# Kernel optimization log

Hardware: AMD Instinct MI355X
Metric: run time of the kernel (lower is better)

The kernel has to match this reference:

```python
import jax, jax.numpy as jnp
import numpy as np

HIDDEN = 896
N_HEADS = 14
N_KV_HEADS = 2
HEAD_DIM = HIDDEN // N_HEADS  # 64
KV_GROUPS = N_HEADS // N_KV_HEADS  # 7
ROPE_THETA = 1000000.0


def rotate_half(x):
    x1, x2 = x[..., : x.shape[-1] // 2], x[..., x.shape[-1] // 2 :]
    return jnp.concatenate((-x2, x1), axis=-1)


def rope_tables(seq_len, dtype=jnp.float32):
    inv_freq = 1.0 / (ROPE_THETA ** (jnp.arange(0, HEAD_DIM, 2, dtype=jnp.float32) / HEAD_DIM))
    t = jnp.arange(seq_len, dtype=jnp.float32)
    freqs = jnp.outer(t, inv_freq)            # [S, D/2]
    emb = jnp.concatenate((freqs, freqs), -1)  # [S, D]
    return jnp.cos(emb).astype(dtype), jnp.sin(emb).astype(dtype)


def setup_inputs() -> dict:
    key = jax.random.key(0)
    ks = jax.random.split(key, 8)
    B, S = 2, 2048
    s = 0.02
    return {
        "hidden_states": jax.random.normal(ks[0], (B, S, HIDDEN), jnp.float32),
        "wq": jax.random.normal(ks[1], (HIDDEN, N_HEADS * HEAD_DIM), jnp.float32) * s,
        "bq": jnp.zeros((N_HEADS * HEAD_DIM,), jnp.float32),
        "wk": jax.random.normal(ks[2], (HIDDEN, N_KV_HEADS * HEAD_DIM), jnp.float32) * s,
        "bk": jnp.zeros((N_KV_HEADS * HEAD_DIM,), jnp.float32),
        "wv": jax.random.normal(ks[3], (HIDDEN, N_KV_HEADS * HEAD_DIM), jnp.float32) * s,
        "bv": jnp.zeros((N_KV_HEADS * HEAD_DIM,), jnp.float32),
        "wo": jax.random.normal(ks[4], (N_HEADS * HEAD_DIM, HIDDEN), jnp.float32) * s,
    }


def reference(hidden_states, wq, bq, wk, bk, wv, bv, wo):
    B, S, _ = hidden_states.shape
    q = (hidden_states @ wq + bq).reshape(B, S, N_HEADS, HEAD_DIM)
    k = (hidden_states @ wk + bk).reshape(B, S, N_KV_HEADS, HEAD_DIM)
    v = (hidden_states @ wv + bv).reshape(B, S, N_KV_HEADS, HEAD_DIM)

    cos, sin = rope_tables(S, hidden_states.dtype)
    cos, sin = cos[None, :, None, :], sin[None, :, None, :]
    q = q * cos + rotate_half(q) * sin
    k = k * cos + rotate_half(k) * sin

    # GQA broadcast: repeat kv heads to match query heads
    k = jnp.repeat(k, KV_GROUPS, axis=2)
    v = jnp.repeat(v, KV_GROUPS, axis=2)

    # [B, H, S, S]
    scores = jnp.einsum("bqhd,bkhd->bhqk", q, k) / jnp.sqrt(jnp.asarray(HEAD_DIM, hidden_states.dtype))
    mask = jnp.tril(jnp.ones((S, S), dtype=jnp.bool_))
    scores = jnp.where(mask[None, None, :, :], scores, jnp.asarray(-1e9, scores.dtype))
    attn = jax.nn.softmax(scores, axis=-1)
    out = jnp.einsum("bhqk,bkhd->bqhd", attn, v).reshape(B, S, N_HEADS * HEAD_DIM)
    return out @ wo
```

## Files before the change

kernel.cpp:

```cpp
#include <hip/hip_runtime.h>

#define HID 896
#define NQ 896
#define NKV 128
#define NQKV 1152
#define NH 14
#define NKVH 2
#define GQ 7
#define DH 64
#define SEQ 2048
#define BATCH 2
#define TOK (BATCH*SEQ)

typedef __attribute__((ext_vector_type(8))) short short8;
typedef __attribute__((ext_vector_type(4))) float f32x4;
typedef __attribute__((ext_vector_type(4))) unsigned short us4;

__device__ __forceinline__ unsigned short f2bf(float x) {
  unsigned int u = __builtin_bit_cast(unsigned int, x);
  u = (u + 0x7fffu + ((u >> 16) & 1u)) >> 16;
  return (unsigned short)u;
}
__device__ __forceinline__ float bf2f(unsigned short b) {
  return __builtin_bit_cast(float, (unsigned int)b << 16);
}
__device__ __forceinline__ f32x4 fzero4() {
  f32x4 z; z[0]=0.f; z[1]=0.f; z[2]=0.f; z[3]=0.f; return z;
}
__device__ __forceinline__ unsigned int cvt_pk_bf16(float lo, float hi) {
  unsigned int r;
  asm("v_cvt_pk_bf16_f32 %0, %1, %2" : "=v"(r) : "v"(lo), "v"(hi));
  return r;
}
__device__ __forceinline__ void gload_lds16(const unsigned short* g, unsigned short* l) {
  __builtin_amdgcn_global_load_lds(
      (const __attribute__((address_space(1))) void*)(const void*)g,
      (__attribute__((address_space(3))) void*)(void*)l, 16, 0, 0);
}

#define CVT_BLKS 3584
#define TRN_BLKS 448
#define BIAS_BLKS 5
#define TAB_BLKS 256
#define PREP_BLKS (CVT_BLKS + TRN_BLKS + BIAS_BLKS + TAB_BLKS)

__global__ void k_prep(const float* __restrict__ hs,
                       const float* __restrict__ wq, const float* __restrict__ bq,
                       const float* __restrict__ wk, const float* __restrict__ bk,
                       const float* __restrict__ wv, const float* __restrict__ bv,
                       const float* __restrict__ wo,
                       unsigned short* __restrict__ hb,
                       unsigned short* __restrict__ wqkvt,
                       unsigned short* __restrict__ wot,
                       float* __restrict__ bqkv,
                       float* __restrict__ ct, float* __restrict__ st) {
  __shared__ unsigned short Ls[64*65];
  int blk = blockIdx.x, tid = threadIdx.x;
  if (blk < CVT_BLKS) {
    int i = blk*256 + tid;
    float4 v = ((const float4*)hs)[i];
    us4 o; o[0]=f2bf(v.x); o[1]=f2bf(v.y); o[2]=f2bf(v.z); o[3]=f2bf(v.w);
    ((us4*)hb)[i] = o;
    return;
  }
  blk -= CVT_BLKS;
  if (blk < TRN_BLKS) {
    const float* W; unsigned short* out; int K, N, n0, k0;
    if (blk < 196)      { W=wq; out=wqkvt;                        K=HID; N=NQ;  int t=blk;     n0=(t%14)*64; k0=(t/14)*64; }
    else if (blk < 224) { W=wk; out=wqkvt + (size_t)NQ*HID;       K=HID; N=NKV; int t=blk-196; n0=(t%2)*64;  k0=(t/2)*64; }
    else if (blk < 252) { W=wv; out=wqkvt + (size_t)(NQ+NKV)*HID; K=HID; N=NKV; int t=blk-224; n0=(t%2)*64;  k0=(t/2)*64; }
    else                { W=wo; out=wot;                          K=NQ;  N=HID; int t=blk-252; n0=(t%14)*64; k0=(t/14)*64; }
    #pragma unroll
    for (int i = 0; i < 16; ++i) {
      int idx = i*256 + tid;
      int r = idx >> 6, c = idx & 63;
      Ls[c*65 + r] = f2bf(W[(size_t)(k0 + r)*N + n0 + c]);
    }
    __syncthreads();
    #pragma unroll
    for (int i = 0; i < 16; ++i) {
      int idx = i*256 + tid;
      int r2 = idx >> 6, c2 = idx & 63;
      out[(size_t)(n0 + r2)*K + k0 + c2] = Ls[r2*65 + c2];
    }
    return;
  }
  blk -= TRN_BLKS;
  if (blk < BIAS_BLKS) {
    int i = blk*256 + tid;
    if (i < NQKV) {
      if (i < NQ) bqkv[i] = bq[i];
      else if (i < NQ + NKV) bqkv[i] = bk[i - NQ];
      else bqkv[i] = bv[i - NQ - NKV];
    }
    return;
  }
  blk -= BIAS_BLKS;
  {
    int i = blk*256 + tid;
    int s = i >> 5, dp = i & 31;
    float inv = __expf(-(float)(2*dp) * (13.815510557964274f / 64.0f));
    float f = (float)s * inv;
    ct[i] = cosf(f); st[i] = sinf(f);
  }
}

template<int OUTMODE>
__global__ __launch_bounds__(256, 2) void k_gemm_bt(
    const unsigned short* __restrict__ A,
    const unsigned short* __restrict__ Bt,
    const float* __restrict__ bias,
    void* __restrict__ Cout,
    int M, int N, int K) {
  __shared__ unsigned short As[128*64];
  __shared__ unsigned short Bs[128*64];
  int tid = threadIdx.x;
  int lane = tid & 63, w = tid >> 6;
  int wr = w >> 1, wc = w & 1;
  int l15 = lane & 15, l4 = lane >> 4;
  int m0 = blockIdx.y * 128, n0 = blockIdx.x * 128;

  f32x4 acc[4][4];
  #pragma unroll
  for (int i = 0; i < 4; ++i)
    #pragma unroll
    for (int j = 0; j < 4; ++j) acc[i][j] = fzero4();

  int nkt = K >> 6;
  for (int kt = 0; kt < nkt; ++kt) {
    int k0 = kt << 6;
    #pragma unroll
    for (int t = 0; t < 4; ++t) {
      int chunk = t*256 + w*64 + lane;
      int row = chunk >> 3, sp = chunk & 7;
      int sl = sp ^ (row & 7);
      gload_lds16(A + (size_t)(m0+row)*K + k0 + sl*8, &As[(t*256 + w*64)*8]);
      gload_lds16(Bt + (size_t)(n0+row)*K + k0 + sl*8, &Bs[(t*256 + w*64)*8]);
    }
    __syncthreads();
    #pragma unroll
    for (int s = 0; s < 2; ++s) {
      short8 af[4], bfr[4];
      #pragma unroll
      for (int mi = 0; mi < 4; ++mi) {
        int row = wr*64 + mi*16 + l15;
        int slot = (s*4 + l4) ^ (row & 7);
        af[mi] = *reinterpret_cast<const short8*>(&As[row*64 + slot*8]);
      }
      #pragma unroll
      for (int ni = 0; ni < 4; ++ni) {
        int row = wc*64 + ni*16 + l15;
        int slot = (s*4 + l4) ^ (row & 7);
        bfr[ni] = *reinterpret_cast<const short8*>(&Bs[row*64 + slot*8]);
      }
      #pragma unroll
      for (int mi = 0; mi < 4; ++mi)
        #pragma unroll
        for (int ni = 0; ni < 4; ++ni)
          acc[mi][ni] = __builtin_amdgcn_mfma_f32_16x16x32_bf16(af[mi], bfr[ni], acc[mi][ni], 0, 0, 0);
    }
    __syncthreads();
  }
  #pragma unroll
  for (int mi = 0; mi < 4; ++mi) {
    #pragma unroll
    for (int ni = 0; ni < 4; ++ni) {
      #pragma unroll
      for (int r = 0; r < 4; ++r) {
        int row = m0 + wr*64 + mi*16 + l4*4 + r;
        int col = n0 + wc*64 + ni*16 + l15;
        float v = acc[mi][ni][r];
        if (OUTMODE == 0) {
          v += bias[col];
          ((unsigned short*)Cout)[(size_t)row*N + col] = f2bf(v);
        } else {
          ((float*)Cout)[(size_t)row*N + col] = v;
        }
      }
    }
  }
}

__global__ void k_rope(const unsigned short* __restrict__ qkv,
                       const float* __restrict__ ct, const float* __restrict__ st,
                       unsigned short* __restrict__ Qr, unsigned short* __restrict__ Kr,
                       unsigned short* __restrict__ Vt) {
  int t = blockIdx.x; int b = t >> 11; int s = t & 2047;
  int tid = threadIdx.x;
  const unsigned short* row = qkv + (size_t)t * NQKV;
  if (tid < 448) {
    int h = tid >> 5, dp = tid & 31;
    float x1 = bf2f(row[h*64 + dp]);
    float x2 = bf2f(row[h*64 + dp + 32]);
    float c = ct[s*32 + dp], sn = st[s*32 + dp];
    size_t base = (((size_t)b*NH + h)*SEQ + s)*64;
    Qr[base + dp]      = f2bf((x1*c - x2*sn) * 0.125f);
    Qr[base + dp + 32] = f2bf((x2*c + x1*sn) * 0.125f);
  } else {
    int j = tid - 448;
    int kvh = j >> 5, dp = j & 31;
    float x1 = bf2f(row[NQ + kvh*64 + dp]);
    float x2 = bf2f(row[NQ + kvh*64 + dp + 32]);
    float c = ct[s*32 + dp], sn = st[s*32 + dp];
    size_t base = (((size_t)b*NKVH + kvh)*SEQ + s)*64;
    Kr[base + dp]      = f2bf(x1*c - x2*sn);
    Kr[base + dp + 32] = f2bf(x2*c + x1*sn);
  }
  if (tid < 128) {
    int kvh = tid >> 6, d = tid & 63;
    Vt[(((size_t)b*NKVH + kvh)*64 + d)*SEQ + s] = row[1024 + kvh*64 + d];
  }
}

__global__ __launch_bounds__(512, 2) void k_attn(
    const unsigned short* __restrict__ Q,
    const unsigned short* __restrict__ Kr,
    const unsigned short* __restrict__ Vt,
    unsigned short* __restrict__ Aout) {
  __shared__ __align__(16) unsigned short Kst[2][64*64];
  __shared__ __align__(16) unsigned short Vst[2][64*64];
  __shared__ __align__(16) unsigned short P_lds[8][16*64];
  int lane = threadIdx.x & 63, w = threadIdx.x >> 6;
  int grp = w >> 2, wsub = w & 3;
  int l15 = lane & 15, l4 = lane >> 4;
  int i = blockIdx.x, h = blockIdx.y, b = blockIdx.z;
  int qtH = 31 - i, qtL = i;
  int qt = grp ? qtL : qtH;
  int kvh = h / GQ;
  const unsigned short* Kb = Kr + ((size_t)(b*NKVH + kvh))*SEQ*64;
  const unsigned short* Vb = Vt + ((size_t)(b*NKVH + kvh))*64*SEQ;
  char* Pw = (char*)&P_lds[w][0];

  auto stage = [&](int kt, int bsel) {
    int chunk = w*64 + lane;
    int row = chunk >> 3;
    int sl = (chunk & 7) ^ (row & 7);
    gload_lds16(Kb + (size_t)(kt*64 + row)*64 + sl*8, &Kst[bsel][chunk*8]);
    gload_lds16(Vb + (size_t)row*SEQ + kt*64 + sl*8, &Vst[bsel][chunk*8]);
  };

  const unsigned short* Qb = Q + (((size_t)(b*NH + h))*SEQ + qt*64 + wsub*16) * 64;
  short8 qa[2];
  #pragma unroll
  for (int s = 0; s < 2; ++s)
    qa[s] = *reinterpret_cast<const short8*>(Qb + l15*64 + s*32 + l4*8);

  f32x4 acc[4];
  #pragma unroll
  for (int n = 0; n < 4; ++n) acc[n] = fzero4();
  float m_run = -__builtin_inff(), l_run = 0.0f;

  stage(0, 0);
  __syncthreads();
  int cur = 0;
  int nkt = qtH + 1;

  for (int kt = 0; kt < nkt; ++kt) {
    if (kt + 1 < nkt) stage(kt + 1, cur ^ 1);
    if (kt <= qt) {
      f32x4 sa[4];
      #pragma unroll
      for (int n = 0; n < 4; ++n) sa[n] = fzero4();
      __builtin_amdgcn_s_setprio(1);
      #pragma unroll
      for (int s = 0; s < 2; ++s) {
        short8 kb[4];
        #pragma unroll
        for (int n = 0; n < 4; ++n) {
          int row = n*16 + l15;
          int slot = (s*4 + l4) ^ (row & 7);
          kb[n] = *reinterpret_cast<const short8*>(&Kst[cur][row*64 + slot*8]);
        }
        #pragma unroll
        for (int n = 0; n < 4; ++n)
          sa[n] = __builtin_amdgcn_mfma_f32_16x16x32_bf16(kb[n], qa[s], sa[n], 0, 0, 0);
      }
      __builtin_amdgcn_s_setprio(0);
      if (kt == qt) {
        int q_glob = qt*64 + wsub*16 + l15;
        #pragma unroll
        for (int n = 0; n < 4; ++n)
          #pragma unroll
          for (int r = 0; r < 4; ++r) {
            int kpos = kt*64 + n*16 + l4*4 + r;
            if (kpos > q_glob) sa[n][r] = -1e30f;
          }
      }
      float t0 = fmaxf(fmaxf(sa[0][0],sa[0][1]), fmaxf(sa[0][2],sa[0][3]));
      float t1 = fmaxf(fmaxf(sa[1][0],sa[1][1]), fmaxf(sa[1][2],sa[1][3]));
      float t2 = fmaxf(fmaxf(sa[2][0],sa[2][1]), fmaxf(sa[2][2],sa[2][3]));
      float t3 = fmaxf(fmaxf(sa[3][0],sa[3][1]), fmaxf(sa[3][2],sa[3][3]));
      float tmax = fmaxf(fmaxf(t0,t1), fmaxf(t2,t3));
      tmax = fmaxf(tmax, __shfl_xor(tmax, 16));
      tmax = fmaxf(tmax, __shfl_xor(tmax, 32));
      float mn = fmaxf(m_run, tmax);
      float sc = __expf(m_run - mn);
      #pragma unroll
      for (int n = 0; n < 4; ++n)
        #pragma unroll
        for (int r = 0; r < 4; ++r) sa[n][r] = __expf(sa[n][r] - mn);
      float s0 = (sa[0][0]+sa[0][1]) + (sa[0][2]+sa[0][3]);
      float s1 = (sa[1][0]+sa[1][1]) + (sa[1][2]+sa[1][3]);
      float s2 = (sa[2][0]+sa[2][1]) + (sa[2][2]+sa[2][3]);
      float s3 = (sa[3][0]+sa[3][1]) + (sa[3][2]+sa[3][3]);
      float sum = (s0+s1) + (s2+s3);
      sum += __shfl_xor(sum, 16);
      sum += __shfl_xor(sum, 32);
      m_run = mn;
      l_run = l_run*sc + sum;
      #pragma unroll
      for (int n = 0; n < 4; ++n) acc[n] *= sc;
      #pragma unroll
      for (int n = 0; n < 4; ++n) {
        uint2 pk;
        pk.x = cvt_pk_bf16(sa[n][0], sa[n][1]);
        pk.y = cvt_pk_bf16(sa[n][2], sa[n][3]);
        int colbyte = n*32 + l4*8;
        int addr = l15*128 + ((((colbyte>>4) ^ (l15&7))) << 4) + (colbyte & 15);
        *reinterpret_cast<uint2*>(Pw + addr) = pk;
      }
      __builtin_amdgcn_s_setprio(1);
      #pragma unroll
      for (int s2i = 0; s2i < 2; ++s2i) {
        int pslot = (s2i*4 + l4) ^ (l15 & 7);
        short8 pa = *reinterpret_cast<const short8*>(Pw + l15*128 + pslot*16);
        #pragma unroll
        for (int n = 0; n < 4; ++n) {
          int row = n*16 + l15;
          int vslot = (s2i*4 + l4) ^ (row & 7);
          short8 vb = *reinterpret_cast<const short8*>(&Vst[cur][row*64 + vslot*8]);
          acc[n] = __builtin_amdgcn_mfma_f32_16x16x32_bf16(vb, pa, acc[n], 0, 0, 0);
        }
      }
      __builtin_amdgcn_s_setprio(0);
    }
    __syncthreads();
    cur ^= 1;
  }

  float inv = 1.0f / l_run;
  #pragma unroll
  for (int n = 0; n < 4; ++n) {
    uint2 pk;
    pk.x = cvt_pk_bf16(acc[n][0]*inv, acc[n][1]*inv);
    pk.y = cvt_pk_bf16(acc[n][2]*inv, acc[n][3]*inv);
    int colbyte = n*32 + l4*8;
    int addr = l15*128 + ((((colbyte>>4) ^ (l15&7))) << 4) + (colbyte & 15);
    *reinterpret_cast<uint2*>(Pw + addr) = pk;
  }
  int row = lane >> 2;
  int cb0 = (lane & 3) * 32;
  #pragma unroll
  for (int it = 0; it < 2; ++it) {
    int cb = cb0 + it*16;
    int slot = (cb >> 4) ^ (row & 7);
    short8 v = *reinterpret_cast<const short8*>(Pw + row*128 + slot*16);
    size_t tok = (size_t)b*SEQ + qt*64 + wsub*16 + row;
    *reinterpret_cast<short8*>(&Aout[tok*NQ + h*64 + (cb>>1)]) = v;
  }
}

extern "C" void kernel_launch(void* const* d_in, const int* in_sizes, int n_in,
                              void* d_out, int out_size, void* d_ws, size_t ws_size,
                              hipStream_t stream) {
  const float* hs = (const float*)d_in[0];
  const float* wq = (const float*)d_in[1];
  const float* bq = (const float*)d_in[2];
  const float* wk = (const float*)d_in[3];
  const float* bk = (const float*)d_in[4];
  const float* wv = (const float*)d_in[5];
  const float* bv = (const float*)d_in[6];
  const float* wo = (const float*)d_in[7];
  float* out = (float*)d_out;

  char* p = (char*)d_ws;
  auto alloc = [&](size_t bytes) { char* r = p; p += (bytes + 255) & ~(size_t)255; return r; };
  unsigned short* hb    = (unsigned short*)alloc((size_t)TOK*HID*2);
  unsigned short* wqkvt = (unsigned short*)alloc((size_t)NQKV*HID*2);
  unsigned short* wot   = (unsigned short*)alloc((size_t)HID*NQ*2);
  float*          bqkv  = (float*)alloc(NQKV*4);
  unsigned short* qkvt  = (unsigned short*)alloc((size_t)TOK*NQKV*2);
  unsigned short* q_r   = (unsigned short*)alloc((size_t)BATCH*NH*SEQ*DH*2);
  unsigned short* k_r   = (unsigned short*)alloc((size_t)BATCH*NKVH*SEQ*DH*2);
  unsigned short* v_t   = (unsigned short*)alloc((size_t)BATCH*NKVH*DH*SEQ*2);
  float*          ct    = (float*)alloc((size_t)SEQ*32*4);
  float*          st    = (float*)alloc((size_t)SEQ*32*4);
  unsigned short* attn  = hb;

  k_prep<<<PREP_BLKS, 256, 0, stream>>>(hs, wq, bq, wk, bk, wv, bv, wo,
                                        hb, wqkvt, wot, bqkv, ct, st);
  k_gemm_bt<0><<<dim3(NQKV/128, TOK/128), 256, 0, stream>>>(hb, wqkvt, bqkv, qkvt, TOK, NQKV, HID);
  k_rope<<<TOK, 512, 0, stream>>>(qkvt, ct, st, q_r, k_r, v_t);
  k_attn<<<dim3(16, NH, BATCH), 512, 0, stream>>>(q_r, k_r, v_t, attn);
  k_gemm_bt<1><<<dim3(NQ/128, TOK/128), 256, 0, stream>>>(attn, wot, nullptr, out, TOK, NQ, HID);
}
```

Baseline: 103.3 us.

## Stage two KV tiles per barrier in attention loop to halve syncs

The attention kernel now loads K/V in slabs of two 64-key tiles per pipeline stage, double-buffered, and processes both tiles between barriers. This halves the number of __syncthreads and makes each prefetch larger, so more work overlaps each global-to-LDS load. In exchange LDS use doubles (K/V buffers go from 32KB to 64KB), which may limit the two blocks per CU implied by the launch bounds. For odd tile counts it also loads one redundant clamped tile.

```diff
diff --git a/kernel.cpp b/kernel.cpp
--- a/kernel.cpp
+++ b/kernel.cpp
@@ -217,8 +217,8 @@
     const unsigned short* __restrict__ Kr,
     const unsigned short* __restrict__ Vt,
     unsigned short* __restrict__ Aout) {
-  __shared__ __align__(16) unsigned short Kst[2][64*64];
-  __shared__ __align__(16) unsigned short Vst[2][64*64];
+  __shared__ __align__(16) unsigned short Kst[2][2][64*64];
+  __shared__ __align__(16) unsigned short Vst[2][2][64*64];
   __shared__ __align__(16) unsigned short P_lds[8][16*64];
   int lane = threadIdx.x & 63, w = threadIdx.x >> 6;
   int grp = w >> 2, wsub = w & 3;
@@ -231,12 +231,16 @@
   const unsigned short* Vb = Vt + ((size_t)(b*NKVH + kvh))*64*SEQ;
   char* Pw = (char*)&P_lds[w][0];
 
-  auto stage = [&](int kt, int bsel) {
-    int chunk = w*64 + lane;
-    int row = chunk >> 3;
-    int sl = (chunk & 7) ^ (row & 7);
-    gload_lds16(Kb + (size_t)(kt*64 + row)*64 + sl*8, &Kst[bsel][chunk*8]);
-    gload_lds16(Vb + (size_t)row*SEQ + kt*64 + sl*8, &Vst[bsel][chunk*8]);
+  auto stage = [&](int slab, int bsel) {
+    #pragma unroll
+    for (int t = 0; t < 2; ++t) {
+      int ks = slab*2 + t; if (ks > 31) ks = 31;
+      int chunk = w*64 + lane;
+      int row = chunk >> 3;
+      int sl = (chunk & 7) ^ (row & 7);
+      gload_lds16(Kb + (size_t)(ks*64 + row)*64 + sl*8, &Kst[bsel][t][chunk*8]);
+      gload_lds16(Vb + (size_t)row*SEQ + ks*64 + sl*8, &Vst[bsel][t][chunk*8]);
+    }
   };
 
   const unsigned short* Qb = Q + (((size_t)(b*NH + h))*SEQ + qt*64 + wsub*16) * 64;
@@ -254,85 +258,92 @@
   __syncthreads();
   int cur = 0;
   int nkt = qtH + 1;
-
-  for (int kt = 0; kt < nkt; ++kt) {
-    if (kt + 1 < nkt) stage(kt + 1, cur ^ 1);
-    if (kt <= qt) {
-      f32x4 sa[4];
-      #pragma unroll
-      for (int n = 0; n < 4; ++n) sa[n] = fzero4();
-      __builtin_amdgcn_s_setprio(1);
-      #pragma unroll
-      for (int s = 0; s < 2; ++s) {
-        short8 kb[4];
-        #pragma unroll
-        for (int n = 0; n < 4; ++n) {
-          int row = n*16 + l15;
-          int slot = (s*4 + l4) ^ (row & 7);
-          kb[n] = *reinterpret_cast<const short8*>(&Kst[cur][row*64 + slot*8]);
+  int nslab = (nkt + 1) >> 1;
+
+  for (int s = 0; s < nslab; ++s) {
+    if (s + 1 < nslab) stage(s + 1, cur ^ 1);
+    #pragma unroll
+    for (int t = 0; t < 2; ++t) {
+      int ks = s*2 + t;
+      if (ks <= qt) {
+        const unsigned short* Ks = &Kst[cur][t][0];
+        const unsigned short* Vs = &Vst[cur][t][0];
+        f32x4 sa[4];
+        #pragma unroll
+        for (int n = 0; n < 4; ++n) sa[n] = fzero4();
+        __builtin_amdgcn_s_setprio(1);
+        #pragma unroll
+        for (int si = 0; si < 2; ++si) {
+          short8 kb[4];
+          #pragma unroll
+          for (int n = 0; n < 4; ++n) {
+            int row = n*16 + l15;
+            int slot = (si*4 + l4) ^ (row & 7);
+            kb[n] = *reinterpret_cast<const short8*>(&Ks[row*64 + slot*8]);
+          }
+          #pragma unroll
+          for (int n = 0; n < 4; ++n)
+            sa[n] = __builtin_amdgcn_mfma_f32_16x16x32_bf16(kb[n], qa[si], sa[n], 0, 0, 0);
         }
-        #pragma unroll
-        for (int n = 0; n < 4; ++n)
-          sa[n] = __builtin_amdgcn_mfma_f32_16x16x32_bf16(kb[n], qa[s], sa[n], 0, 0, 0);
-      }
-      __builtin_amdgcn_s_setprio(0);
-      if (kt == qt) {
-        int q_glob = qt*64 + wsub*16 + l15;
+        __builtin_amdgcn_s_setprio(0);
+        if (ks == qt) {
+          int q_glob = qt*64 + wsub*16 + l15;
+          #pragma unroll
+          for (int n = 0; n < 4; ++n)
+            #pragma unroll
+            for (int r = 0; r < 4; ++r) {
+              int kpos = ks*64 + n*16 + l4*4 + r;
+              if (kpos > q_glob) sa[n][r] = -1e30f;
+            }
+        }
+        float t0 = fmaxf(fmaxf(sa[0][0],sa[0][1]), fmaxf(sa[0][2],sa[0][3]));
+        float t1 = fmaxf(fmaxf(sa[1][0],sa[1][1]), fmaxf(sa[1][2],sa[1][3]));
+        float t2 = fmaxf(fmaxf(sa[2][0],sa[2][1]), fmaxf(sa[2][2],sa[2][3]));
+        float t3 = fmaxf(fmaxf(sa[3][0],sa[3][1]), fmaxf(sa[3][2],sa[3][3]));
+        float tmax = fmaxf(fmaxf(t0,t1), fmaxf(t2,t3));
+        tmax = fmaxf(tmax, __shfl_xor(tmax, 16));
+        tmax = fmaxf(tmax, __shfl_xor(tmax, 32));
+        float mn = fmaxf(m_run, tmax);
+        float sc = __expf(m_run - mn);
         #pragma unroll
         for (int n = 0; n < 4; ++n)
           #pragma unroll
-          for (int r = 0; r < 4; ++r) {
-            int kpos = kt*64 + n*16 + l4*4 + r;
-            if (kpos > q_glob) sa[n][r] = -1e30f;
+          for (int r = 0; r < 4; ++r) sa[n][r] = __expf(sa[n][r] - mn);
+        float s0 = (sa[0][0]+sa[0][1]) + (sa[0][2]+sa[0][3]);
+        float s1 = (sa[1][0]+sa[1][1]) + (sa[1][2]+sa[1][3]);
+        float s2 = (sa[2][0]+sa[2][1]) + (sa[2][2]+sa[2][3]);
+        float s3 = (sa[3][0]+sa[3][1]) + (sa[3][2]+sa[3][3]);
+        float sum = (s0+s1) + (s2+s3);
+        sum += __shfl_xor(sum, 16);
+        sum += __shfl_xor(sum, 32);
+        m_run = mn;
+        l_run = l_run*sc + sum;
+        #pragma unroll
+        for (int n = 0; n < 4; ++n) acc[n] *= sc;
+        #pragma unroll
+        for (int n = 0; n < 4; ++n) {
+          uint2 pk;
+          pk.x = cvt_pk_bf16(sa[n][0], sa[n][1]);
+          pk.y = cvt_pk_bf16(sa[n][2], sa[n][3]);
+          int colbyte = n*32 + l4*8;
+          int addr = l15*128 + ((((colbyte>>4) ^ (l15&7))) << 4) + (colbyte & 15);
+          *reinterpret_cast<uint2*>(Pw + addr) = pk;
+        }
+        __builtin_amdgcn_s_setprio(1);
+        #pragma unroll
+        for (int s2i = 0; s2i < 2; ++s2i) {
+          int pslot = (s2i*4 + l4) ^ (l15 & 7);
+          short8 pa = *reinterpret_cast<const short8*>(Pw + l15*128 + pslot*16);
+          #pragma unroll
+          for (int n = 0; n < 4; ++n) {
+            int row = n*16 + l15;
+            int vslot = (s2i*4 + l4) ^ (row & 7);
+            short8 vb = *reinterpret_cast<const short8*>(&Vs[row*64 + vslot*8]);
+            acc[n] = __builtin_amdgcn_mfma_f32_16x16x32_bf16(vb, pa, acc[n], 0, 0, 0);
           }
+        }
+        __builtin_amdgcn_s_setprio(0);
       }
-      float t0 = fmaxf(fmaxf(sa[0][0],sa[0][1]), fmaxf(sa[0][2],sa[0][3]));
-      float t1 = fmaxf(fmaxf(sa[1][0],sa[1][1]), fmaxf(sa[1][2],sa[1][3]));
-      float t2 = fmaxf(fmaxf(sa[2][0],sa[2][1]), fmaxf(sa[2][2],sa[2][3]));
-      float t3 = fmaxf(fmaxf(sa[3][0],sa[3][1]), fmaxf(sa[3][2],sa[3][3]));
-      float tmax = fmaxf(fmaxf(t0,t1), fmaxf(t2,t3));
-      tmax = fmaxf(tmax, __shfl_xor(tmax, 16));
-      tmax = fmaxf(tmax, __shfl_xor(tmax, 32));
-      float mn = fmaxf(m_run, tmax);
-      float sc = __expf(m_run - mn);
-      #pragma unroll
-      for (int n = 0; n < 4; ++n)
-        #pragma unroll
-        for (int r = 0; r < 4; ++r) sa[n][r] = __expf(sa[n][r] - mn);
-      float s0 = (sa[0][0]+sa[0][1]) + (sa[0][2]+sa[0][3]);
-      float s1 = (sa[1][0]+sa[1][1]) + (sa[1][2]+sa[1][3]);
-      float s2 = (sa[2][0]+sa[2][1]) + (sa[2][2]+sa[2][3]);
-      float s3 = (sa[3][0]+sa[3][1]) + (sa[3][2]+sa[3][3]);
-      float sum = (s0+s1) + (s2+s3);
-      sum += __shfl_xor(sum, 16);
-      sum += __shfl_xor(sum, 32);
-      m_run = mn;
-      l_run = l_run*sc + sum;
-      #pragma unroll
-      for (int n = 0; n < 4; ++n) acc[n] *= sc;
-      #pragma unroll
-      for (int n = 0; n < 4; ++n) {
-        uint2 pk;
-        pk.x = cvt_pk_bf16(sa[n][0], sa[n][1]);
-        pk.y = cvt_pk_bf16(sa[n][2], sa[n][3]);
-        int colbyte = n*32 + l4*8;
-        int addr = l15*128 + ((((colbyte>>4) ^ (l15&7))) << 4) + (colbyte & 15);
-        *reinterpret_cast<uint2*>(Pw + addr) = pk;
-      }
-      __builtin_amdgcn_s_setprio(1);
-      #pragma unroll
-      for (int s2i = 0; s2i < 2; ++s2i) {
-        int pslot = (s2i*4 + l4) ^ (l15 & 7);
-        short8 pa = *reinterpret_cast<const short8*>(Pw + l15*128 + pslot*16);
-        #pragma unroll
-        for (int n = 0; n < 4; ++n) {
-          int row = n*16 + l15;
-          int vslot = (s2i*4 + l4) ^ (row & 7);
-          short8 vb = *reinterpret_cast<const short8*>(&Vst[cur][row*64 + vslot*8]);
-          acc[n] = __builtin_amdgcn_mfma_f32_16x16x32_bf16(vb, pa, acc[n], 0, 0, 0);
-        }
-      }
-      __builtin_amdgcn_s_setprio(0);
     }
     __syncthreads();
     cur ^= 1;
```

New measurement: 102.0 us. No clear change (-1.2%).
